# Kernel tuning notes

Measured on AMD Instinct MI355X. Metric: run time of the kernel, lower is better.

Reference implementation:

```python
import jax, jax.numpy as jnp
import numpy as np

IN_, OUT_, HID, B = 1024, 1024, 4, 8192

def setup_inputs() -> dict:
    key = jax.random.key(0)
    k_x, k_w1, k_b1, k_w2, k_b2 = jax.random.split(key, 5)
    x = jax.random.normal(k_x, (B, IN_), dtype=jnp.float32)
    # Stacked params for out_ tiny MLPs: Linear(in,4) -> LeakyReLU(0.1) -> Linear(4,1)
    s1 = 1.0 / np.sqrt(IN_)
    s2 = 1.0 / np.sqrt(HID)
    W1 = jax.random.uniform(k_w1, (OUT_, IN_, HID), dtype=jnp.float32, minval=-s1, maxval=s1)
    b1 = jax.random.uniform(k_b1, (OUT_, HID), dtype=jnp.float32, minval=-s1, maxval=s1)
    W2 = jax.random.uniform(k_w2, (OUT_, HID), dtype=jnp.float32, minval=-s2, maxval=s2)
    b2 = jax.random.uniform(k_b2, (OUT_,), dtype=jnp.float32, minval=-s2, maxval=s2)
    return {"x": x, "W1": W1, "b1": b1, "W2": W2, "b2": b2}

def reference(x, W1, b1, W2, b2):
    # h[b,o,h] = x[b,:] @ W1[o] + b1[o]  (shared input across all out_ MLPs)
    h = jnp.einsum('bi,oih->boh', x, W1) + b1
    h = jnp.where(h >= 0, h, 0.1 * h)  # LeakyReLU(0.1)
    # out[b,o] = h[b,o,:] @ W2[o] + b2[o]; equals torch.cat of per-MLP scalars
    out = jnp.einsum('boh,oh->bo', h, W2) + b2
    return out
```

## Files before the change

kernel.cpp:

```cpp
#include <hip/hip_runtime.h>
#include <hip/hip_bf16.h>

#define IN_DIM  1024
#define OUT_DIM 1024
#define HID     4
#define BATCH   8192
#define NCOL    (OUT_DIM * HID)

typedef __bf16 bf16x8 __attribute__((ext_vector_type(8)));
typedef float  f32x4  __attribute__((ext_vector_type(4)));

__device__ __forceinline__ unsigned short f2bf(float f) {
  union { float f; unsigned int u; } v; v.f = f;
  unsigned int u = v.u;
  u += 0x7FFFu + ((u >> 16) & 1u);
  return (unsigned short)(u >> 16);
}

__global__ __launch_bounds__(256) void cvt_x_kernel(const float4* __restrict__ in,
                                                    ushort4* __restrict__ out) {
  int i = blockIdx.x * 256 + threadIdx.x;
  float4 v = in[i];
  ushort4 o;
  o.x = f2bf(v.x); o.y = f2bf(v.y); o.z = f2bf(v.z); o.w = f2bf(v.w);
  out[i] = o;
}

__global__ __launch_bounds__(256) void cvt_w1t_kernel(const float* __restrict__ W1,
                                                      ushort4* __restrict__ out) {
  int b = blockIdx.x;
  int g = ((b & 7) * ((int)gridDim.x >> 3) + (b >> 3)) * 256 + threadIdx.x;
  int i4 = g & 255;
  int oh = g >> 8;
  int h = oh & 3, o = oh >> 2;
  const float* src = W1 + (size_t)o * 4096 + h;
  ushort4 r;
  r.x = f2bf(src[(i4 * 4 + 0) * 4]);
  r.y = f2bf(src[(i4 * 4 + 1) * 4]);
  r.z = f2bf(src[(i4 * 4 + 2) * 4]);
  r.w = f2bf(src[(i4 * 4 + 3) * 4]);
  out[(size_t)oh * 256 + i4] = r;
}

__device__ __forceinline__ void gload16(const void* g, void* l) {
  __builtin_amdgcn_global_load_lds(
      (const __attribute__((address_space(1))) unsigned int*)g,
      (__attribute__((address_space(3))) unsigned int*)l, 16, 0, 0);
}

__global__ __launch_bounds__(256, 2) void mlp_gemm_kernel(
    const unsigned short* __restrict__ A,
    const unsigned short* __restrict__ Bm,
    const f32x4* __restrict__ b1v,
    const f32x4* __restrict__ w2v,
    const float* __restrict__ b2,
    float* __restrict__ out) {
  __shared__ __align__(16) unsigned short lds[36864];

  const int bid = blockIdx.x;
  const int xcd = bid & 7, loc = bid >> 3;
  const int bm = loc >> 3;
  const int bn = xcd * 8 + (loc & 7);
  const int tileM = bm * 256, tileN = bn * 128;

  const int t = threadIdx.x;
  const int lane = t & 63, wid = t >> 6;
  const int wm = wid >> 1, wn = wid & 1;
  const int frow = lane & 15, jq = lane >> 4;

  const int sr = t >> 2;
  const int sc = (((t & 3) ^ (sr & 3)) << 3);
  const unsigned short* Abase = A  + (size_t)(tileM + sr) * IN_DIM + sc;
  const unsigned short* Bbase = Bm + (size_t)(tileN + sr) * IN_DIM + sc;

  auto stage = [&](int kt, int p) {
    const int kb = kt * 32;
    unsigned short* lA = lds + p * 12288 + t * 8;
#pragma unroll
    for (int i = 0; i < 4; ++i)
      gload16(Abase + (size_t)i * 64 * IN_DIM + kb, lA + i * 2048);
#pragma unroll
    for (int i = 0; i < 2; ++i)
      gload16(Bbase + (size_t)i * 64 * IN_DIM + kb, lA + 8192 + i * 2048);
  };

  const f32x4 fzero = {0.f, 0.f, 0.f, 0.f};
  f32x4 acc[8][4];
#pragma unroll
  for (int m = 0; m < 8; ++m)
#pragma unroll
    for (int n = 0; n < 4; ++n) acc[m][n] = fzero;

  const int pslot = (jq ^ (frow & 3)) << 3;
  const int aoff = (wm * 128 + frow) * 32 + pslot;
  const int boff = 8192 + (wn * 64 + frow) * 32 + pslot;

  stage(0, 0);
  stage(1, 1);
  asm volatile("s_waitcnt vmcnt(6)" ::: "memory");
  __builtin_amdgcn_s_barrier();

  auto ktile = [&](int kt, int pr, int ps, int mode) {
    if (mode == 0) stage(kt + 2, ps);
    const unsigned short* bufp = lds + pr * 12288;
    bf16x8 af[8], bfr[4];
#pragma unroll
    for (int mf = 0; mf < 8; ++mf)
      af[mf] = *(const bf16x8*)(bufp + aoff + mf * 512);
#pragma unroll
    for (int nf = 0; nf < 4; ++nf)
      bfr[nf] = *(const bf16x8*)(bufp + boff + nf * 512);
    asm volatile("s_waitcnt lgkmcnt(0)" ::: "memory");
    __builtin_amdgcn_sched_barrier(0);
    __builtin_amdgcn_s_setprio(1);
#pragma unroll
    for (int mf = 0; mf < 8; ++mf)
#pragma unroll
      for (int nf = 0; nf < 4; ++nf)
        acc[mf][nf] = __builtin_amdgcn_mfma_f32_16x16x32_bf16(af[mf], bfr[nf], acc[mf][nf], 0, 0, 0);
    __builtin_amdgcn_s_setprio(0);
    if (mode == 0)      asm volatile("s_waitcnt vmcnt(6)" ::: "memory");
    else if (mode == 1) asm volatile("s_waitcnt vmcnt(0)" ::: "memory");
    __builtin_amdgcn_s_barrier();
  };

  for (int g = 0; g < 30; g += 3) {
    ktile(g,     0, 2, 0);
    ktile(g + 1, 1, 0, 0);
    ktile(g + 2, 2, 1, 0);
  }
  ktile(30, 0, 0, 1);
  ktile(31, 1, 0, 2);

  float* LE = (float*)lds;
  const int obase = tileM >> 2;
#pragma unroll
  for (int mf = 0; mf < 8; ++mf) {
    int o_loc = wm * 32 + mf * 4 + jq;
    f32x4 b1q = b1v[obase + o_loc];
    f32x4 w2q = w2v[obase + o_loc];
#pragma unroll
    for (int nf = 0; nf < 4; ++nf) {
      int bat = wn * 64 + nf * 16 + frow;
      f32x4 q = acc[mf][nf];
      float v = 0.f;
#pragma unroll
      for (int j = 0; j < 4; ++j) {
        float hj = q[j] + b1q[j];
        hj = (hj >= 0.f) ? hj : 0.1f * hj;
        v += hj * w2q[j];
      }
      LE[bat * 68 + o_loc] = v;
    }
  }
  __builtin_amdgcn_s_barrier();

  const int col = t & 63, rowb = t >> 6;
  const float b2s = b2[obase + col];
  float* outB = out + (size_t)tileN * OUT_DIM + obase;
#pragma unroll
  for (int i = 0; i < 32; ++i) {
    int row = rowb + i * 4;
    outB[(size_t)row * OUT_DIM + col] = LE[row * 68 + col] + b2s;
  }
}

__global__ __launch_bounds__(256) void fallback_kernel(
    const float* __restrict__ x, const float* __restrict__ W1,
    const float* __restrict__ b1, const float* __restrict__ W2,
    const float* __restrict__ b2, float* __restrict__ out) {
  int idx = blockIdx.x * 256 + threadIdx.x;
  if (idx >= BATCH * OUT_DIM) return;
  int bb = idx >> 10, o = idx & 1023;
  const float4* w1p = (const float4*)(W1 + (size_t)o * 4096);
  const float*  xp  = x + (size_t)bb * 1024;
  float4 acc = *(const float4*)(b1 + o * 4);
  for (int i = 0; i < 1024; ++i) {
    float xv = xp[i];
    float4 w = w1p[i];
    acc.x += xv * w.x; acc.y += xv * w.y; acc.z += xv * w.z; acc.w += xv * w.w;
  }
  float4 w2 = *(const float4*)(W2 + o * 4);
  float r = b2[o];
  r += ((acc.x >= 0.f) ? acc.x : 0.1f * acc.x) * w2.x;
  r += ((acc.y >= 0.f) ? acc.y : 0.1f * acc.y) * w2.y;
  r += ((acc.z >= 0.f) ? acc.z : 0.1f * acc.z) * w2.z;
  r += ((acc.w >= 0.f) ? acc.w : 0.1f * acc.w) * w2.w;
  out[(size_t)bb * OUT_DIM + o] = r;
}

extern "C" void kernel_launch(void* const* d_in, const int* in_sizes, int n_in,
                              void* d_out, int out_size, void* d_ws, size_t ws_size,
                              hipStream_t stream) {
  const float* x  = (const float*)d_in[0];
  const float* W1 = (const float*)d_in[1];
  const float* b1 = (const float*)d_in[2];
  const float* W2 = (const float*)d_in[3];
  const float* b2 = (const float*)d_in[4];
  float* out = (float*)d_out;

  size_t need = (size_t)BATCH * IN_DIM * 2 + (size_t)NCOL * IN_DIM * 2;
  if (ws_size >= need) {
    unsigned short* xbf = (unsigned short*)d_ws;
    unsigned short* w1t = xbf + (size_t)BATCH * IN_DIM;
    cvt_x_kernel<<<(BATCH * IN_DIM / 4) / 256, 256, 0, stream>>>((const float4*)x, (ushort4*)xbf);
    cvt_w1t_kernel<<<(NCOL * IN_DIM / 4) / 256, 256, 0, stream>>>(W1, (ushort4*)w1t);
    mlp_gemm_kernel<<<(NCOL / 256) * (BATCH / 128), 256, 0, stream>>>(
        w1t, xbf, (const f32x4*)b1, (const f32x4*)W2, b2, out);
  } else {
    fallback_kernel<<<(BATCH * OUT_DIM + 255) / 256, 256, 0, stream>>>(x, W1, b1, W2, b2, out);
  }
}
```

Measured before the change: 91.42 us.

## Switch GEMM main loop to 32x32x16 bf16 MFMA with new LDS swizzle

Replaces the 16x16x32 MFMA tiling (8x4 fragments per wave) with 32x32x16 MFMA (4x2 fragments, two k-halves per tile). This cuts the number of LDS fragment reads and MFMA issues per k-tile. The LDS swizzle and the epilogue mapping change to match the 32-row fragment layout, and the epilogue stride moves to 65. The explicit lgkmcnt wait and setprio are dropped in favour of compiler scheduling, which may weaken the load/compute interleave.

```diff
diff --git a/kernel.cpp b/kernel.cpp
--- a/kernel.cpp
+++ b/kernel.cpp
@@ -9,6 +9,7 @@
 
 typedef __bf16 bf16x8 __attribute__((ext_vector_type(8)));
 typedef float  f32x4  __attribute__((ext_vector_type(4)));
+typedef float  f32x16 __attribute__((ext_vector_type(16)));
 
 __device__ __forceinline__ unsigned short f2bf(float f) {
   union { float f; unsigned int u; } v; v.f = f;
@@ -66,10 +67,10 @@
   const int t = threadIdx.x;
   const int lane = t & 63, wid = t >> 6;
   const int wm = wid >> 1, wn = wid & 1;
-  const int frow = lane & 15, jq = lane >> 4;
+  const int l31 = lane & 31, hi = lane >> 5;
 
   const int sr = t >> 2;
-  const int sc = (((t & 3) ^ (sr & 3)) << 3);
+  const int sc = (((t & 3) ^ ((sr >> 1) & 3)) << 3);
   const unsigned short* Abase = A  + (size_t)(tileM + sr) * IN_DIM + sc;
   const unsigned short* Bbase = Bm + (size_t)(tileN + sr) * IN_DIM + sc;
 
@@ -84,44 +85,58 @@
       gload16(Bbase + (size_t)i * 64 * IN_DIM + kb, lA + 8192 + i * 2048);
   };
 
-  const f32x4 fzero = {0.f, 0.f, 0.f, 0.f};
-  f32x4 acc[8][4];
-#pragma unroll
-  for (int m = 0; m < 8; ++m)
-#pragma unroll
-    for (int n = 0; n < 4; ++n) acc[m][n] = fzero;
-
-  const int pslot = (jq ^ (frow & 3)) << 3;
-  const int aoff = (wm * 128 + frow) * 32 + pslot;
-  const int boff = 8192 + (wn * 64 + frow) * 32 + pslot;
+  f32x16 acc[4][2];
+#pragma unroll
+  for (int m = 0; m < 4; ++m)
+#pragma unroll
+    for (int n = 0; n < 2; ++n)
+#pragma unroll
+      for (int r = 0; r < 16; ++r) acc[m][n][r] = 0.f;
+
+  const int swz = (l31 >> 1) & 3;
+  const int p0 = (hi ^ swz) * 8;
+  const int p1 = ((2 + hi) ^ swz) * 8;
+  const int arow = (wm * 128 + l31) * 32;
+  const int brow = 8192 + (wn * 64 + l31) * 32;
 
   stage(0, 0);
   stage(1, 1);
   asm volatile("s_waitcnt vmcnt(6)" ::: "memory");
   __builtin_amdgcn_s_barrier();
+  __builtin_amdgcn_sched_barrier(0);
 
   auto ktile = [&](int kt, int pr, int ps, int mode) {
     if (mode == 0) stage(kt + 2, ps);
     const unsigned short* bufp = lds + pr * 12288;
-    bf16x8 af[8], bfr[4];
-#pragma unroll
-    for (int mf = 0; mf < 8; ++mf)
-      af[mf] = *(const bf16x8*)(bufp + aoff + mf * 512);
-#pragma unroll
-    for (int nf = 0; nf < 4; ++nf)
-      bfr[nf] = *(const bf16x8*)(bufp + boff + nf * 512);
-    asm volatile("s_waitcnt lgkmcnt(0)" ::: "memory");
-    __builtin_amdgcn_sched_barrier(0);
-    __builtin_amdgcn_s_setprio(1);
-#pragma unroll
-    for (int mf = 0; mf < 8; ++mf)
-#pragma unroll
-      for (int nf = 0; nf < 4; ++nf)
-        acc[mf][nf] = __builtin_amdgcn_mfma_f32_16x16x32_bf16(af[mf], bfr[nf], acc[mf][nf], 0, 0, 0);
-    __builtin_amdgcn_s_setprio(0);
+    bf16x8 a0[4], b0[2], a1[4], b1_[2];
+    a0[0] = *(const bf16x8*)(bufp + arow + 0 * 1024 + p0);
+    b0[0] = *(const bf16x8*)(bufp + brow + 0 * 1024 + p0);
+    b0[1] = *(const bf16x8*)(bufp + brow + 1 * 1024 + p0);
+    a0[1] = *(const bf16x8*)(bufp + arow + 1 * 1024 + p0);
+    a0[2] = *(const bf16x8*)(bufp + arow + 2 * 1024 + p0);
+    a0[3] = *(const bf16x8*)(bufp + arow + 3 * 1024 + p0);
+    a1[0] = *(const bf16x8*)(bufp + arow + 0 * 1024 + p1);
+    b1_[0] = *(const bf16x8*)(bufp + brow + 0 * 1024 + p1);
+    b1_[1] = *(const bf16x8*)(bufp + brow + 1 * 1024 + p1);
+    a1[1] = *(const bf16x8*)(bufp + arow + 1 * 1024 + p1);
+    a1[2] = *(const bf16x8*)(bufp + arow + 2 * 1024 + p1);
+    a1[3] = *(const bf16x8*)(bufp + arow + 3 * 1024 + p1);
+#pragma unroll
+    for (int mf = 0; mf < 4; ++mf)
+#pragma unroll
+      for (int nf = 0; nf < 2; ++nf)
+        acc[mf][nf] = __builtin_amdgcn_mfma_f32_32x32x16_bf16(a0[mf], b0[nf], acc[mf][nf], 0, 0, 0);
+#pragma unroll
+    for (int mf = 0; mf < 4; ++mf)
+#pragma unroll
+      for (int nf = 0; nf < 2; ++nf)
+        acc[mf][nf] = __builtin_amdgcn_mfma_f32_32x32x16_bf16(a1[mf], b1_[nf], acc[mf][nf], 0, 0, 0);
     if (mode == 0)      asm volatile("s_waitcnt vmcnt(6)" ::: "memory");
     else if (mode == 1) asm volatile("s_waitcnt vmcnt(0)" ::: "memory");
-    __builtin_amdgcn_s_barrier();
+    if (mode < 2) {
+      __builtin_amdgcn_s_barrier();
+      __builtin_amdgcn_sched_barrier(0);
+    }
   };
 
   for (int g = 0; g < 30; g += 3) {
@@ -131,29 +146,32 @@
   }
   ktile(30, 0, 0, 1);
   ktile(31, 1, 0, 2);
+  __syncthreads();
 
   float* LE = (float*)lds;
   const int obase = tileM >> 2;
 #pragma unroll
-  for (int mf = 0; mf < 8; ++mf) {
-    int o_loc = wm * 32 + mf * 4 + jq;
-    f32x4 b1q = b1v[obase + o_loc];
-    f32x4 w2q = w2v[obase + o_loc];
-#pragma unroll
-    for (int nf = 0; nf < 4; ++nf) {
-      int bat = wn * 64 + nf * 16 + frow;
-      f32x4 q = acc[mf][nf];
-      float v = 0.f;
-#pragma unroll
-      for (int j = 0; j < 4; ++j) {
-        float hj = q[j] + b1q[j];
-        hj = (hj >= 0.f) ? hj : 0.1f * hj;
-        v += hj * w2q[j];
+  for (int mf = 0; mf < 4; ++mf) {
+#pragma unroll
+    for (int g = 0; g < 4; ++g) {
+      int o_loc = wm * 32 + mf * 8 + 2 * g + hi;
+      f32x4 b1q = b1v[obase + o_loc];
+      f32x4 w2q = w2v[obase + o_loc];
+#pragma unroll
+      for (int nf = 0; nf < 2; ++nf) {
+        int bat = wn * 64 + nf * 32 + l31;
+        float v = 0.f;
+#pragma unroll
+        for (int h = 0; h < 4; ++h) {
+          float hj = acc[mf][nf][4 * g + h] + b1q[h];
+          hj = (hj >= 0.f) ? hj : 0.1f * hj;
+          v += hj * w2q[h];
+        }
+        LE[bat * 65 + o_loc] = v;
       }
-      LE[bat * 68 + o_loc] = v;
     }
   }
-  __builtin_amdgcn_s_barrier();
+  __syncthreads();
 
   const int col = t & 63, rowb = t >> 6;
   const float b2s = b2[obase + col];
@@ -161,7 +179,7 @@
 #pragma unroll
   for (int i = 0; i < 32; ++i) {
     int row = rowb + i * 4;
-    outB[(size_t)row * OUT_DIM + col] = LE[row * 68 + col] + b2s;
+    outB[(size_t)row * OUT_DIM + col] = LE[row * 65 + col] + b2s;
   }
 }
 
```

Measured after the change: 95.36 us. +4.3%, slower.
